# Performance work log

Hardware: AMD Instinct MI355X
Metric: run time of the kernel (lower is better)

Reference implementation:

```python
import jax, jax.numpy as jnp
import numpy as np

NUM_HEADS = 8


def setup_inputs() -> dict:
    key = jax.random.key(0)
    ks = jax.random.split(key, 8)
    B, C, H, W = 8, 512, 64, 64
    s = 1.0 / np.sqrt(C)
    return {
        "guide": jax.random.normal(ks[0], (B, C), dtype=jnp.float32),
        "hidden_rep": jax.random.normal(ks[1], (B, C, H, W), dtype=jnp.float32),
        "Wq": jax.random.normal(ks[2], (C, C), dtype=jnp.float32) * s,
        "bq": jnp.zeros((C,), dtype=jnp.float32),
        "Wk": jax.random.normal(ks[3], (C, C), dtype=jnp.float32) * s,
        "bk": jnp.zeros((C,), dtype=jnp.float32),
        "Wv": jax.random.normal(ks[4], (C, C), dtype=jnp.float32) * s,
        "bv": jnp.zeros((C,), dtype=jnp.float32),
    }


def reference(guide, hidden_rep, Wq, bq, Wk, bk, Wv, bv):
    B, C, H, W = hidden_rep.shape
    nh = NUM_HEADS
    d = C // nh
    scale = 1.0 / (d ** 0.5)

    # hidden_rep: [B,C,H,W] -> [B, HW, C] (token-major, matching torch permute+reshape)
    hr = hidden_rep.transpose(0, 2, 3, 1).reshape(B, H * W, C)

    # guide is broadcast identically over all HW positions in the original;
    # the linear commutes with the broadcast, so compute once then broadcast.
    q_row = guide @ Wq.T + bq                                   # [B, C]
    q_tok = jnp.broadcast_to(q_row[:, None, :], (B, H * W, C))  # [B, HW, C]
    k_tok = hr @ Wk.T + bk                                      # [B, HW, C]
    v_tok = hr @ Wv.T + bv                                      # [B, HW, C]

    # Faithful replication of torch split_heads: view [B,HW,C] as [B,nh,d,H,W]
    # (this scrambles spatial/channel axes exactly as the original does),
    # then permute to [B, nh, H, W, d].
    def split_heads(x):
        return x.reshape(B, nh, d, H, W).transpose(0, 1, 3, 4, 2)

    q = split_heads(q_tok)  # [B, nh, H, W, d]
    k = split_heads(k_tok)
    v = split_heads(v_tok)

    # Row-wise attention: softmax over the width axis only.
    scores = jnp.einsum('bnhqd,bnhkd->bnhqk', q, k) * scale  # [B, nh, H, W, W]
    weights = jax.nn.softmax(scores, axis=-1)
    attended = jnp.einsum('bnhqk,bnhkd->bnhqd', weights, v)  # [B, nh, H, W, d]

    # permute(0,1,4,2,3) -> [B, nh, d, H, W] -> [B, C, H, W]
    return attended.transpose(0, 1, 4, 2, 3).reshape(B, C, H, W)
```

## Files before the change

kernel.cpp:

```cpp
#include <hip/hip_runtime.h>
#include <hip/hip_bf16.h>
#include <stdint.h>


typedef __attribute__((ext_vector_type(8))) short bf16x8_t;
typedef __attribute__((ext_vector_type(4))) float f32x4_t;

__device__ __forceinline__ unsigned short f2bf(float f) {
  unsigned int u = __float_as_uint(f);
  u += 0x7FFFu + ((u >> 16) & 1u);
  return (unsigned short)(u >> 16);
}

__device__ __forceinline__ void gload16(const void* g, void* lds) {
  __builtin_amdgcn_global_load_lds(
      (const __attribute__((address_space(1))) unsigned int*)g,
      (__attribute__((address_space(3))) unsigned int*)lds, 16, 0, 0);
}

__global__ __launch_bounds__(256) void k_trans(const float* __restrict__ hid,
                                               unsigned short* __restrict__ XT,
                                               float* __restrict__ hrsum,
                                               const float* __restrict__ Wv,
                                               unsigned short* __restrict__ Wvb) {
  int bid = blockIdx.x;
  int tid = threadIdx.x;
  if (bid >= 1024) {
    int blk = bid - 1024;
#pragma unroll
    for (int i = 0; i < 16; ++i) {
      int idx = blk * 4096 + i * 256 + tid;
      float4 v = ((const float4*)Wv)[idx];
      ushort4 o;
      o.x = f2bf(v.x); o.y = f2bf(v.y); o.z = f2bf(v.z); o.w = f2bf(v.w);
      ((ushort4*)Wvb)[idx] = o;
    }
    return;
  }
  int rh = bid & 1, cb = (bid >> 1) & 7, n = (bid >> 4) & 7, b = bid >> 7;
  __shared__ float T[32][65];
  __shared__ float hsred[32][8];
  ((float*)hsred)[tid] = 0.f;

  float part[2][4];
#pragma unroll
  for (int m = 0; m < 2; ++m)
#pragma unroll
    for (int i = 0; i < 4; ++i) part[m][i] = 0.f;

  const int f4 = tid & 15;
  const int r0 = tid >> 4;
  const float* srcbase = hid + (size_t)(b * 512 + cb * 64 + rh * 32) * 4096 + n * 512;
  unsigned short* xtbase =
      XT + (size_t)(b * 8 + n) * 512 * 512 + cb * 64 + rh * 32;

  float4 va[2], vb2[2];
#pragma unroll
  for (int m = 0; m < 2; ++m)
    va[m] = *(const float4*)(srcbase + (size_t)(r0 + 16 * m) * 4096 + f4 * 4);

#define TSTEP(JC, CUR, NXT, LAST)                                              \
  do {                                                                         \
    _Pragma("unroll")                                                          \
    for (int m_ = 0; m_ < 2; ++m_) {                                           \
      int r_ = r0 + 16 * m_;                                                   \
      T[r_][f4 * 4 + 0] = CUR[m_].x;  T[r_][f4 * 4 + 1] = CUR[m_].y;           \
      T[r_][f4 * 4 + 2] = CUR[m_].z;  T[r_][f4 * 4 + 3] = CUR[m_].w;           \
      part[m_][0] += CUR[m_].x; part[m_][1] += CUR[m_].y;                      \
      part[m_][2] += CUR[m_].z; part[m_][3] += CUR[m_].w;                      \
    }                                                                          \
    if (!(LAST)) {                                                             \
      _Pragma("unroll")                                                        \
      for (int m_ = 0; m_ < 2; ++m_)                                           \
        NXT[m_] = *(const float4*)(srcbase + (size_t)(r0 + 16 * m_) * 4096 +   \
                                   ((JC) + 1) * 64 + f4 * 4);                  \
    }                                                                          \
    __syncthreads();                                                           \
    {                                                                          \
      int jl_ = tid >> 2, o_ = tid & 3;                                        \
      unsigned short t0 = f2bf(T[o_ * 8 + 0][jl_]);                            \
      unsigned short t1 = f2bf(T[o_ * 8 + 1][jl_]);                            \
      unsigned short t2 = f2bf(T[o_ * 8 + 2][jl_]);                            \
      unsigned short t3 = f2bf(T[o_ * 8 + 3][jl_]);                            \
      unsigned short t4 = f2bf(T[o_ * 8 + 4][jl_]);                            \
      unsigned short t5 = f2bf(T[o_ * 8 + 5][jl_]);                            \
      unsigned short t6 = f2bf(T[o_ * 8 + 6][jl_]);                            \
      unsigned short t7 = f2bf(T[o_ * 8 + 7][jl_]);                            \
      uint4 pk_;                                                               \
      pk_.x = (unsigned)t0 | ((unsigned)t1 << 16);                             \
      pk_.y = (unsigned)t2 | ((unsigned)t3 << 16);                             \
      pk_.z = (unsigned)t4 | ((unsigned)t5 << 16);                             \
      pk_.w = (unsigned)t6 | ((unsigned)t7 << 16);                             \
      *(uint4*)(xtbase + (size_t)((JC) * 64 + jl_) * 512 + o_ * 8) = pk_;      \
    }                                                                          \
    __syncthreads();                                                           \
  } while (0)

  TSTEP(0, va, vb2, 0);
  TSTEP(1, vb2, va, 0);
  TSTEP(2, va, vb2, 0);
  TSTEP(3, vb2, va, 0);
  TSTEP(4, va, vb2, 0);
  TSTEP(5, vb2, va, 0);
  TSTEP(6, va, vb2, 0);
  TSTEP(7, vb2, va, 1);
#undef TSTEP

  {
    int gbase = (f4 & 1) * 4;
#pragma unroll
    for (int m = 0; m < 2; ++m) {
      int r = r0 + 16 * m;
#pragma unroll
      for (int i = 0; i < 4; ++i) atomicAdd(&hsred[r][gbase + i], part[m][i]);
    }
  }
  __syncthreads();
  float* hout = hrsum + (size_t)(b * 8 + n) * 4096 + cb * 64 + rh * 32;
  {
    int g = tid >> 5, r = tid & 31;
    hout[(size_t)g * 512 + r] = hsred[r][g];
  }
}

__global__ __launch_bounds__(256) void k_k2(const float* __restrict__ hrsum,
                                            const float* __restrict__ Wk,
                                            const float* __restrict__ bk,
                                            const float* __restrict__ guide,
                                            const float* __restrict__ Wq,
                                            const float* __restrict__ bq,
                                            float* __restrict__ K2,
                                            float* __restrict__ qs) {
  int bid = blockIdx.x;
  int rt = bid >> 4, ct = bid & 15;
  bool isQ = (rt == 16);
  const float* A = isQ ? guide : (hrsum + (size_t)rt * 32 * 512);
  const float* Bm = isQ ? Wq : Wk;
  int arows = isQ ? 8 : 32;
  int tid = threadIdx.x;
  __shared__ float Ah[32][36];
  __shared__ float Bh[32][36];
  int r = tid >> 3, f = tid & 7;
  int oy = (tid >> 4) * 2, ox = (tid & 15) * 2;
  float a00 = 0.f, a01 = 0.f, a10 = 0.f, a11 = 0.f;

  for (int kc = 0; kc < 16; ++kc) {
    __syncthreads();
    float4 av = (r < arows) ? *(const float4*)(A + (size_t)r * 512 + kc * 32 + f * 4)
                            : make_float4(0.f, 0.f, 0.f, 0.f);
    *(float4*)(&Ah[r][f * 4]) = av;
    float4 bv = *(const float4*)(Bm + (size_t)(ct * 32 + r) * 512 + kc * 32 + f * 4);
    *(float4*)(&Bh[r][f * 4]) = bv;
    __syncthreads();
#pragma unroll
    for (int kk = 0; kk < 32; kk += 4) {
      float4 x0 = *(float4*)(&Ah[oy][kk]);
      float4 x1 = *(float4*)(&Ah[oy + 1][kk]);
      float4 y0 = *(float4*)(&Bh[ox][kk]);
      float4 y1 = *(float4*)(&Bh[ox + 1][kk]);
      a00 += x0.x * y0.x + x0.y * y0.y + x0.z * y0.z + x0.w * y0.w;
      a01 += x0.x * y1.x + x0.y * y1.y + x0.z * y1.z + x0.w * y1.w;
      a10 += x1.x * y0.x + x1.y * y0.y + x1.z * y0.z + x1.w * y0.w;
      a11 += x1.x * y1.x + x1.y * y1.y + x1.z * y1.z + x1.w * y1.w;
    }
  }
  int c0 = ct * 32 + ox;
  if (!isQ) {
    int row0 = rt * 32 + oy;
    K2[(size_t)row0 * 512 + c0]           = a00 + 64.f * bk[c0];
    K2[(size_t)row0 * 512 + c0 + 1]       = a01 + 64.f * bk[c0 + 1];
    K2[(size_t)(row0 + 1) * 512 + c0]     = a10 + 64.f * bk[c0];
    K2[(size_t)(row0 + 1) * 512 + c0 + 1] = a11 + 64.f * bk[c0 + 1];
  } else if (oy < 8) {
    const float scale = 0.125f;
    qs[(size_t)oy * 512 + c0]           = (a00 + bq[c0]) * scale;
    qs[(size_t)oy * 512 + c0 + 1]       = (a01 + bq[c0 + 1]) * scale;
    qs[(size_t)(oy + 1) * 512 + c0]     = (a10 + bq[c0]) * scale;
    qs[(size_t)(oy + 1) * 512 + c0 + 1] = (a11 + bq[c0 + 1]) * scale;
  }
}

__global__ __launch_bounds__(512, 4) void k_fused(
    const unsigned short* __restrict__ XT, const unsigned short* __restrict__ Wvb,
    const float* __restrict__ K2, const float* __restrict__ qs,
    const float* __restrict__ bv, float* __restrict__ out) {
  int p = blockIdx.x;
  int xcd = p & 7, idx = p >> 3;
  int slab = xcd * 8 + (idx & 7);
  int g = idx >> 3;
  int n = slab & 7, b = slab >> 3;

  int tid = threadIdx.x;
  int w = tid >> 6, l = tid & 63;
  int l15 = l & 15, l4 = l >> 4, lr = l >> 3, lc = l & 7;

  __shared__ __align__(16) unsigned char smem[65536];

  const unsigned swzel = (unsigned)((lc ^ lr) << 3);
  const unsigned short* bsrc = XT + (size_t)slab * 512 * 512;
  const unsigned short* wbase = Wvb + (size_t)(w * 64 + l15) * 512 + l4 * 8;
  const int brow = 8 * (w * 8 + lr) + g;

#pragma unroll
  for (int i = 0; i < 8; ++i)
    gload16(bsrc + (size_t)brow * 512 + i * 64 + swzel, smem + i * 8192 + w * 1024);

  float alpha = qs[(size_t)b * 512 + w * 64 + l];
  float beta  = K2[(size_t)(slab * 8 + g) * 512 + w * 64 + l];
  float bvreg = bv[w * 64 + l];

  f32x4_t acc[4][4];
#pragma unroll
  for (int i = 0; i < 4; ++i)
#pragma unroll
    for (int j = 0; j < 4; ++j) acc[i][j] = (f32x4_t){0.f, 0.f, 0.f, 0.f};

  __syncthreads();

#pragma unroll
  for (int s = 0; s < 16; ++s) {
    bf16x8_t af[4];
#pragma unroll
    for (int mt = 0; mt < 4; ++mt)
      af[mt] = *(const bf16x8_t*)(wbase + mt * 16 * 512 + s * 32);
    unsigned char* Bb = smem + (s >> 1) * 8192;
    bf16x8_t bfr[4];
#pragma unroll
    for (int nt = 0; nt < 4; ++nt) {
      unsigned row = (unsigned)(nt * 16 + l15);
      bfr[nt] = *(const bf16x8_t*)(Bb + row * 128 +
                ((unsigned)((s & 1) * 64 + l4 * 16) ^ ((row & 7) << 4)));
    }
    __builtin_amdgcn_s_setprio(1);
#pragma unroll
    for (int mt = 0; mt < 4; ++mt)
#pragma unroll
      for (int nt = 0; nt < 4; ++nt)
        acc[mt][nt] = __builtin_amdgcn_mfma_f32_16x16x32_bf16(
            af[mt], bfr[nt], acc[mt][nt], 0, 0, 0);
    __builtin_amdgcn_s_setprio(0);
  }

  __syncthreads();

  unsigned char* Vp = smem + w * 8192;
#pragma unroll
  for (int mt = 0; mt < 4; ++mt) {
    float bq0 = __shfl(bvreg, mt * 16 + l4 * 4 + 0);
    float bq1 = __shfl(bvreg, mt * 16 + l4 * 4 + 1);
    float bq2 = __shfl(bvreg, mt * 16 + l4 * 4 + 2);
    float bq3 = __shfl(bvreg, mt * 16 + l4 * 4 + 3);
#pragma unroll
    for (int nt = 0; nt < 4; ++nt) {
      unsigned dd = (unsigned)(nt * 16 + l15);
      uint2 pk;
      pk.x = (unsigned)f2bf(acc[mt][nt][0] + bq0) |
             ((unsigned)f2bf(acc[mt][nt][1] + bq1) << 16);
      pk.y = (unsigned)f2bf(acc[mt][nt][2] + bq2) |
             ((unsigned)f2bf(acc[mt][nt][3] + bq3) << 16);
      *(uint2*)(Vp + dd * 128 +
                ((unsigned)(mt * 32 + l4 * 8) ^ ((dd & 7) << 4))) = pk;
    }
  }

  float bmax = beta, bmin = beta;
#pragma unroll
  for (int o = 32; o >= 1; o >>= 1) {
    bmax = fmaxf(bmax, __shfl_xor(bmax, o));
    bmin = fminf(bmin, __shfl_xor(bmin, o));
  }
  float m = alpha >= 0.f ? alpha * bmax : alpha * bmin;
  float ssum = 0.f;
#pragma unroll 8
  for (int kk = 0; kk < 64; ++kk)
    ssum += __expf(fmaf(alpha, __shfl(beta, kk), -m));
  float inv = 1.0f / ssum;

  f32x4_t acc2[4][4];
#pragma unroll
  for (int i = 0; i < 4; ++i)
#pragma unroll
    for (int j = 0; j < 4; ++j) acc2[i][j] = (f32x4_t){0.f, 0.f, 0.f, 0.f};

#pragma unroll
  for (int ks = 0; ks < 2; ++ks) {
    bf16x8_t va[4];
#pragma unroll
    for (int mt = 0; mt < 4; ++mt) {
      unsigned dd = (unsigned)(mt * 16 + l15);
      va[mt] = *(const bf16x8_t*)(Vp + dd * 128 +
                ((unsigned)(ks * 64 + l4 * 16) ^ ((dd & 7) << 4)));
    }
    float bvv[8];
#pragma unroll
    for (int i = 0; i < 8; ++i) bvv[i] = __shfl(beta, ks * 32 + l4 * 8 + i);
    bf16x8_t pb[4];
#pragma unroll
    for (int nt = 0; nt < 4; ++nt) {
      int qq = nt * 16 + l15;
      float aq = __shfl(alpha, qq);
      float mq = __shfl(m, qq);
      float iq = __shfl(inv, qq);
      bf16x8_t pp;
#pragma unroll
      for (int i = 0; i < 8; ++i)
        pp[i] = (short)f2bf(__expf(fmaf(aq, bvv[i], -mq)) * iq);
      pb[nt] = pp;
    }
#pragma unroll
    for (int mt = 0; mt < 4; ++mt)
#pragma unroll
      for (int nt = 0; nt < 4; ++nt)
        acc2[mt][nt] = __builtin_amdgcn_mfma_f32_16x16x32_bf16(
            va[mt], pb[nt], acc2[mt][nt], 0, 0, 0);
  }

#pragma unroll
  for (int mt = 0; mt < 4; ++mt) {
#pragma unroll
    for (int r = 0; r < 4; ++r) {
      int dd = mt * 16 + l4 * 4 + r;
      size_t base = (((size_t)(b * 512 + n * 64 + dd)) * 64 + (g * 8 + w)) * 64;
#pragma unroll
      for (int nt = 0; nt < 4; ++nt)
        out[base + nt * 16 + l15] = acc2[mt][nt][r];
    }
  }
}

extern "C" void kernel_launch(void* const* d_in, const int* in_sizes, int n_in,
                              void* d_out, int out_size, void* d_ws, size_t ws_size,
                              hipStream_t stream) {
  const float* guide = (const float*)d_in[0];
  const float* hid   = (const float*)d_in[1];
  const float* Wq    = (const float*)d_in[2];
  const float* bq    = (const float*)d_in[3];
  const float* Wk    = (const float*)d_in[4];
  const float* bk    = (const float*)d_in[5];
  const float* Wv    = (const float*)d_in[6];
  const float* bv    = (const float*)d_in[7];
  float* out = (float*)d_out;

  char* ws = (char*)d_ws;
  unsigned short* XT  = (unsigned short*)(ws);
  unsigned short* Wvb = (unsigned short*)(ws + 33554432);
  float* hrsum        = (float*)(ws + 34078720);
  float* K2           = (float*)(ws + 35127296);
  float* qs           = (float*)(ws + 36175872);

  k_trans<<<1040, 256, 0, stream>>>(hid, XT, hrsum, Wv, Wvb);
  k_k2<<<272, 256, 0, stream>>>(hrsum, Wk, bk, guide, Wq, bq, K2, qs);
  k_fused<<<512, 512, 0, stream>>>(XT, Wvb, K2, qs, bv, out);
}
```

Before: 94.70 us.

## Precompute softmax probability matrix in separate kernel and double-buffer weight loads

```diff
diff --git a/kernel.cpp b/kernel.cpp
--- a/kernel.cpp
+++ b/kernel.cpp
@@ -180,10 +180,58 @@
   }
 }
 
+__global__ __launch_bounds__(512) void k_pmat(const float* __restrict__ K2,
+                                              const float* __restrict__ qs,
+                                              unsigned short* __restrict__ P) {
+  int p = blockIdx.x;
+  int slab = p >> 3, g = p & 7;
+  int b = slab >> 3;
+  int tid = threadIdx.x;
+  int w = tid >> 6, l = tid & 63;
+
+  float alpha = qs[(size_t)b * 512 + w * 64 + l];
+  float beta  = K2[(size_t)(slab * 8 + g) * 512 + w * 64 + l];
+
+  float bmax = beta, bmin = beta;
+#pragma unroll
+  for (int o = 32; o >= 1; o >>= 1) {
+    bmax = fmaxf(bmax, __shfl_xor(bmax, o));
+    bmin = fminf(bmin, __shfl_xor(bmin, o));
+  }
+  float m = alpha >= 0.f ? alpha * bmax : alpha * bmin;
+  float ssum = 0.f;
+#pragma unroll 8
+  for (int kk = 0; kk < 64; ++kk)
+    ssum += __expf(fmaf(alpha, __shfl(beta, kk), -m));
+  float inv = 1.0f / ssum;
+
+  unsigned short* Pb = P + (((size_t)(slab * 8 + g)) * 8 + w) * 4096;
+  const int qrow = l >> 3, koff = (l & 7) * 8;
+#pragma unroll
+  for (int p8 = 0; p8 < 8; ++p8) {
+    int qq = p8 * 8 + qrow;
+    float aq = __shfl(alpha, qq);
+    float mq = __shfl(m, qq);
+    float iq = __shfl(inv, qq);
+    unsigned short v[8];
+#pragma unroll
+    for (int i = 0; i < 8; ++i) {
+      float bk = __shfl(beta, koff + i);
+      v[i] = f2bf(__expf(fmaf(aq, bk, -mq)) * iq);
+    }
+    uint4 pk;
+    pk.x = (unsigned)v[0] | ((unsigned)v[1] << 16);
+    pk.y = (unsigned)v[2] | ((unsigned)v[3] << 16);
+    pk.z = (unsigned)v[4] | ((unsigned)v[5] << 16);
+    pk.w = (unsigned)v[6] | ((unsigned)v[7] << 16);
+    *(uint4*)(Pb + qq * 64 + koff) = pk;
+  }
+}
+
 __global__ __launch_bounds__(512, 4) void k_fused(
     const unsigned short* __restrict__ XT, const unsigned short* __restrict__ Wvb,
-    const float* __restrict__ K2, const float* __restrict__ qs,
-    const float* __restrict__ bv, float* __restrict__ out) {
+    const unsigned short* __restrict__ P, const float* __restrict__ bv,
+    float* __restrict__ out) {
   int p = blockIdx.x;
   int xcd = p & 7, idx = p >> 3;
   int slab = xcd * 8 + (idx & 7);
@@ -205,8 +253,6 @@
   for (int i = 0; i < 8; ++i)
     gload16(bsrc + (size_t)brow * 512 + i * 64 + swzel, smem + i * 8192 + w * 1024);
 
-  float alpha = qs[(size_t)b * 512 + w * 64 + l];
-  float beta  = K2[(size_t)(slab * 8 + g) * 512 + w * 64 + l];
   float bvreg = bv[w * 64 + l];
 
   f32x4_t acc[4][4];
@@ -217,12 +263,19 @@
 
   __syncthreads();
 
+  bf16x8_t af[2][4];
+#pragma unroll
+  for (int mt = 0; mt < 4; ++mt)
+    af[0][mt] = *(const bf16x8_t*)(wbase + mt * 16 * 512);
+
 #pragma unroll
   for (int s = 0; s < 16; ++s) {
-    bf16x8_t af[4];
-#pragma unroll
-    for (int mt = 0; mt < 4; ++mt)
-      af[mt] = *(const bf16x8_t*)(wbase + mt * 16 * 512 + s * 32);
+    if (s < 15) {
+#pragma unroll
+      for (int mt = 0; mt < 4; ++mt)
+        af[(s + 1) & 1][mt] =
+            *(const bf16x8_t*)(wbase + mt * 16 * 512 + (s + 1) * 32);
+    }
     unsigned char* Bb = smem + (s >> 1) * 8192;
     bf16x8_t bfr[4];
 #pragma unroll
@@ -231,15 +284,21 @@
       bfr[nt] = *(const bf16x8_t*)(Bb + row * 128 +
                 ((unsigned)((s & 1) * 64 + l4 * 16) ^ ((row & 7) << 4)));
     }
-    __builtin_amdgcn_s_setprio(1);
 #pragma unroll
     for (int mt = 0; mt < 4; ++mt)
 #pragma unroll
       for (int nt = 0; nt < 4; ++nt)
         acc[mt][nt] = __builtin_amdgcn_mfma_f32_16x16x32_bf16(
-            af[mt], bfr[nt], acc[mt][nt], 0, 0, 0);
-    __builtin_amdgcn_s_setprio(0);
-  }
+            af[s & 1][mt], bfr[nt], acc[mt][nt], 0, 0, 0);
+  }
+
+  const unsigned short* Pb = P + (((size_t)(slab * 8 + g)) * 8 + w) * 4096;
+  bf16x8_t pb[2][4];
+#pragma unroll
+  for (int ks = 0; ks < 2; ++ks)
+#pragma unroll
+    for (int nt = 0; nt < 4; ++nt)
+      pb[ks][nt] = *(const bf16x8_t*)(Pb + (nt * 16 + l15) * 64 + ks * 32 + l4 * 8);
 
   __syncthreads();
 
@@ -263,19 +322,6 @@
     }
   }
 
-  float bmax = beta, bmin = beta;
-#pragma unroll
-  for (int o = 32; o >= 1; o >>= 1) {
-    bmax = fmaxf(bmax, __shfl_xor(bmax, o));
-    bmin = fminf(bmin, __shfl_xor(bmin, o));
-  }
-  float m = alpha >= 0.f ? alpha * bmax : alpha * bmin;
-  float ssum = 0.f;
-#pragma unroll 8
-  for (int kk = 0; kk < 64; ++kk)
-    ssum += __expf(fmaf(alpha, __shfl(beta, kk), -m));
-  float inv = 1.0f / ssum;
-
   f32x4_t acc2[4][4];
 #pragma unroll
   for (int i = 0; i < 4; ++i)
@@ -291,28 +337,12 @@
       va[mt] = *(const bf16x8_t*)(Vp + dd * 128 +
                 ((unsigned)(ks * 64 + l4 * 16) ^ ((dd & 7) << 4)));
     }
-    float bvv[8];
-#pragma unroll
-    for (int i = 0; i < 8; ++i) bvv[i] = __shfl(beta, ks * 32 + l4 * 8 + i);
-    bf16x8_t pb[4];
-#pragma unroll
-    for (int nt = 0; nt < 4; ++nt) {
-      int qq = nt * 16 + l15;
-      float aq = __shfl(alpha, qq);
-      float mq = __shfl(m, qq);
-      float iq = __shfl(inv, qq);
-      bf16x8_t pp;
-#pragma unroll
-      for (int i = 0; i < 8; ++i)
-        pp[i] = (short)f2bf(__expf(fmaf(aq, bvv[i], -mq)) * iq);
-      pb[nt] = pp;
-    }
 #pragma unroll
     for (int mt = 0; mt < 4; ++mt)
 #pragma unroll
       for (int nt = 0; nt < 4; ++nt)
         acc2[mt][nt] = __builtin_amdgcn_mfma_f32_16x16x32_bf16(
-            va[mt], pb[nt], acc2[mt][nt], 0, 0, 0);
+            va[mt], pb[ks][nt], acc2[mt][nt], 0, 0, 0);
   }
 
 #pragma unroll
@@ -347,8 +377,10 @@
   float* hrsum        = (float*)(ws + 34078720);
   float* K2           = (float*)(ws + 35127296);
   float* qs           = (float*)(ws + 36175872);
+  unsigned short* P   = (unsigned short*)(ws + 36192256);
 
   k_trans<<<1040, 256, 0, stream>>>(hid, XT, hrsum, Wv, Wvb);
   k_k2<<<272, 256, 0, stream>>>(hrsum, Wk, bk, guide, Wq, bq, K2, qs);
-  k_fused<<<512, 512, 0, stream>>>(XT, Wvb, K2, qs, bv, out);
-}
+  k_pmat<<<512, 512, 0, stream>>>(K2, qs, P);
+  k_fused<<<512, 512, 0, stream>>>(XT, Wvb, P, bv, out);
+}
```

New measurement: 108.5 us. 1.15x slower.

## Process two head slabs per fused block to reuse Wv fragments

Applied to the files above, without the earlier changes.

```diff
diff --git a/kernel.cpp b/kernel.cpp
--- a/kernel.cpp
+++ b/kernel.cpp
@@ -180,152 +180,183 @@
   }
 }
 
-__global__ __launch_bounds__(512, 4) void k_fused(
+__global__ __launch_bounds__(512, 2) void k_fused(
     const unsigned short* __restrict__ XT, const unsigned short* __restrict__ Wvb,
     const float* __restrict__ K2, const float* __restrict__ qs,
     const float* __restrict__ bv, float* __restrict__ out) {
   int p = blockIdx.x;
   int xcd = p & 7, idx = p >> 3;
-  int slab = xcd * 8 + (idx & 7);
-  int g = idx >> 3;
-  int n = slab & 7, b = slab >> 3;
+  int sp = xcd * 4 + (idx & 3);
+  int g = idx >> 2;
+  int slab0 = sp * 2, slab1 = slab0 + 1;
+  int b = sp >> 2;
+  int n0 = slab0 & 7, n1 = slab1 & 7;
 
   int tid = threadIdx.x;
   int w = tid >> 6, l = tid & 63;
   int l15 = l & 15, l4 = l >> 4, lr = l >> 3, lc = l & 7;
 
-  __shared__ __align__(16) unsigned char smem[65536];
+  __shared__ __align__(16) unsigned char smem[131072];
 
   const unsigned swzel = (unsigned)((lc ^ lr) << 3);
-  const unsigned short* bsrc = XT + (size_t)slab * 512 * 512;
+  const unsigned short* xsrc0 = XT + (size_t)slab0 * 512 * 512;
+  const unsigned short* xsrc1 = XT + (size_t)slab1 * 512 * 512;
   const unsigned short* wbase = Wvb + (size_t)(w * 64 + l15) * 512 + l4 * 8;
   const int brow = 8 * (w * 8 + lr) + g;
 
 #pragma unroll
   for (int i = 0; i < 8; ++i)
-    gload16(bsrc + (size_t)brow * 512 + i * 64 + swzel, smem + i * 8192 + w * 1024);
+    gload16(xsrc0 + (size_t)brow * 512 + i * 64 + swzel,
+            smem + i * 8192 + w * 1024);
+#pragma unroll
+  for (int i = 0; i < 8; ++i)
+    gload16(xsrc1 + (size_t)brow * 512 + i * 64 + swzel,
+            smem + 65536 + i * 8192 + w * 1024);
 
   float alpha = qs[(size_t)b * 512 + w * 64 + l];
-  float beta  = K2[(size_t)(slab * 8 + g) * 512 + w * 64 + l];
+  float beta0 = K2[(size_t)(slab0 * 8 + g) * 512 + w * 64 + l];
+  float beta1 = K2[(size_t)(slab1 * 8 + g) * 512 + w * 64 + l];
   float bvreg = bv[w * 64 + l];
 
-  f32x4_t acc[4][4];
+  f32x4_t acc0[4][4], acc1[4][4];
 #pragma unroll
   for (int i = 0; i < 4; ++i)
 #pragma unroll
-    for (int j = 0; j < 4; ++j) acc[i][j] = (f32x4_t){0.f, 0.f, 0.f, 0.f};
+    for (int j = 0; j < 4; ++j) {
+      acc0[i][j] = (f32x4_t){0.f, 0.f, 0.f, 0.f};
+      acc1[i][j] = (f32x4_t){0.f, 0.f, 0.f, 0.f};
+    }
 
   __syncthreads();
 
+  bf16x8_t af[2][4];
+#pragma unroll
+  for (int mt = 0; mt < 4; ++mt)
+    af[0][mt] = *(const bf16x8_t*)(wbase + mt * 16 * 512);
+
 #pragma unroll
   for (int s = 0; s < 16; ++s) {
-    bf16x8_t af[4];
-#pragma unroll
-    for (int mt = 0; mt < 4; ++mt)
-      af[mt] = *(const bf16x8_t*)(wbase + mt * 16 * 512 + s * 32);
-    unsigned char* Bb = smem + (s >> 1) * 8192;
-    bf16x8_t bfr[4];
+    if (s < 15) {
+#pragma unroll
+      for (int mt = 0; mt < 4; ++mt)
+        af[(s + 1) & 1][mt] =
+            *(const bf16x8_t*)(wbase + mt * 16 * 512 + (s + 1) * 32);
+    }
+    unsigned colx = (unsigned)((s & 1) * 64 + l4 * 16);
+    unsigned char* Ba = smem + (s >> 1) * 8192;
+    unsigned char* Bb = smem + 65536 + (s >> 1) * 8192;
+    bf16x8_t b0[4], b1[4];
 #pragma unroll
     for (int nt = 0; nt < 4; ++nt) {
       unsigned row = (unsigned)(nt * 16 + l15);
-      bfr[nt] = *(const bf16x8_t*)(Bb + row * 128 +
-                ((unsigned)((s & 1) * 64 + l4 * 16) ^ ((row & 7) << 4)));
-    }
-    __builtin_amdgcn_s_setprio(1);
+      unsigned off = row * 128 + (colx ^ ((row & 7) << 4));
+      b0[nt] = *(const bf16x8_t*)(Ba + off);
+      b1[nt] = *(const bf16x8_t*)(Bb + off);
+    }
 #pragma unroll
     for (int mt = 0; mt < 4; ++mt)
 #pragma unroll
       for (int nt = 0; nt < 4; ++nt)
-        acc[mt][nt] = __builtin_amdgcn_mfma_f32_16x16x32_bf16(
-            af[mt], bfr[nt], acc[mt][nt], 0, 0, 0);
-    __builtin_amdgcn_s_setprio(0);
+        acc0[mt][nt] = __builtin_amdgcn_mfma_f32_16x16x32_bf16(
+            af[s & 1][mt], b0[nt], acc0[mt][nt], 0, 0, 0);
+#pragma unroll
+    for (int mt = 0; mt < 4; ++mt)
+#pragma unroll
+      for (int nt = 0; nt < 4; ++nt)
+        acc1[mt][nt] = __builtin_amdgcn_mfma_f32_16x16x32_bf16(
+            af[s & 1][mt], b1[nt], acc1[mt][nt], 0, 0, 0);
   }
 
   __syncthreads();
 
-  unsigned char* Vp = smem + w * 8192;
-#pragma unroll
-  for (int mt = 0; mt < 4; ++mt) {
-    float bq0 = __shfl(bvreg, mt * 16 + l4 * 4 + 0);
-    float bq1 = __shfl(bvreg, mt * 16 + l4 * 4 + 1);
-    float bq2 = __shfl(bvreg, mt * 16 + l4 * 4 + 2);
-    float bq3 = __shfl(bvreg, mt * 16 + l4 * 4 + 3);
-#pragma unroll
-    for (int nt = 0; nt < 4; ++nt) {
-      unsigned dd = (unsigned)(nt * 16 + l15);
-      uint2 pk;
-      pk.x = (unsigned)f2bf(acc[mt][nt][0] + bq0) |
-             ((unsigned)f2bf(acc[mt][nt][1] + bq1) << 16);
-      pk.y = (unsigned)f2bf(acc[mt][nt][2] + bq2) |
-             ((unsigned)f2bf(acc[mt][nt][3] + bq3) << 16);
-      *(uint2*)(Vp + dd * 128 +
-                ((unsigned)(mt * 32 + l4 * 8) ^ ((dd & 7) << 4))) = pk;
-    }
-  }
-
-  float bmax = beta, bmin = beta;
-#pragma unroll
-  for (int o = 32; o >= 1; o >>= 1) {
-    bmax = fmaxf(bmax, __shfl_xor(bmax, o));
-    bmin = fminf(bmin, __shfl_xor(bmin, o));
-  }
-  float m = alpha >= 0.f ? alpha * bmax : alpha * bmin;
-  float ssum = 0.f;
-#pragma unroll 8
-  for (int kk = 0; kk < 64; ++kk)
-    ssum += __expf(fmaf(alpha, __shfl(beta, kk), -m));
-  float inv = 1.0f / ssum;
-
-  f32x4_t acc2[4][4];
-#pragma unroll
-  for (int i = 0; i < 4; ++i)
-#pragma unroll
-    for (int j = 0; j < 4; ++j) acc2[i][j] = (f32x4_t){0.f, 0.f, 0.f, 0.f};
-
-#pragma unroll
-  for (int ks = 0; ks < 2; ++ks) {
-    bf16x8_t va[4];
-#pragma unroll
-    for (int mt = 0; mt < 4; ++mt) {
-      unsigned dd = (unsigned)(mt * 16 + l15);
-      va[mt] = *(const bf16x8_t*)(Vp + dd * 128 +
-                ((unsigned)(ks * 64 + l4 * 16) ^ ((dd & 7) << 4)));
-    }
-    float bvv[8];
-#pragma unroll
-    for (int i = 0; i < 8; ++i) bvv[i] = __shfl(beta, ks * 32 + l4 * 8 + i);
-    bf16x8_t pb[4];
-#pragma unroll
-    for (int nt = 0; nt < 4; ++nt) {
-      int qq = nt * 16 + l15;
-      float aq = __shfl(alpha, qq);
-      float mq = __shfl(m, qq);
-      float iq = __shfl(inv, qq);
-      bf16x8_t pp;
-#pragma unroll
-      for (int i = 0; i < 8; ++i)
-        pp[i] = (short)f2bf(__expf(fmaf(aq, bvv[i], -mq)) * iq);
-      pb[nt] = pp;
-    }
-#pragma unroll
-    for (int mt = 0; mt < 4; ++mt)
-#pragma unroll
-      for (int nt = 0; nt < 4; ++nt)
-        acc2[mt][nt] = __builtin_amdgcn_mfma_f32_16x16x32_bf16(
-            va[mt], pb[nt], acc2[mt][nt], 0, 0, 0);
-  }
-
-#pragma unroll
-  for (int mt = 0; mt < 4; ++mt) {
-#pragma unroll
-    for (int r = 0; r < 4; ++r) {
-      int dd = mt * 16 + l4 * 4 + r;
-      size_t base = (((size_t)(b * 512 + n * 64 + dd)) * 64 + (g * 8 + w)) * 64;
-#pragma unroll
-      for (int nt = 0; nt < 4; ++nt)
-        out[base + nt * 16 + l15] = acc2[mt][nt][r];
-    }
-  }
+#define SLAB_TAIL(ACC, VPOFF, BETA, NN)                                        \
+  do {                                                                         \
+    unsigned char* Vp = smem + (VPOFF) + w * 8192;                             \
+    _Pragma("unroll")                                                          \
+    for (int mt = 0; mt < 4; ++mt) {                                           \
+      float bq0 = __shfl(bvreg, mt * 16 + l4 * 4 + 0);                         \
+      float bq1 = __shfl(bvreg, mt * 16 + l4 * 4 + 1);                         \
+      float bq2 = __shfl(bvreg, mt * 16 + l4 * 4 + 2);                         \
+      float bq3 = __shfl(bvreg, mt * 16 + l4 * 4 + 3);                         \
+      _Pragma("unroll")                                                        \
+      for (int nt = 0; nt < 4; ++nt) {                                         \
+        unsigned dd = (unsigned)(nt * 16 + l15);                               \
+        uint2 pk;                                                              \
+        pk.x = (unsigned)f2bf(ACC[mt][nt][0] + bq0) |                          \
+               ((unsigned)f2bf(ACC[mt][nt][1] + bq1) << 16);                   \
+        pk.y = (unsigned)f2bf(ACC[mt][nt][2] + bq2) |                          \
+               ((unsigned)f2bf(ACC[mt][nt][3] + bq3) << 16);                   \
+        *(uint2*)(Vp + dd * 128 +                                              \
+                  ((unsigned)(mt * 32 + l4 * 8) ^ ((dd & 7) << 4))) = pk;      \
+      }                                                                        \
+    }                                                                          \
+    float bmax = (BETA), bmin = (BETA);                                        \
+    _Pragma("unroll")                                                          \
+    for (int o = 32; o >= 1; o >>= 1) {                                        \
+      bmax = fmaxf(bmax, __shfl_xor(bmax, o));                                 \
+      bmin = fminf(bmin, __shfl_xor(bmin, o));                                 \
+    }                                                                          \
+    float m = alpha >= 0.f ? alpha * bmax : alpha * bmin;                      \
+    float ssum = 0.f;                                                          \
+    _Pragma("unroll 8")                                                        \
+    for (int kk = 0; kk < 64; ++kk)                                            \
+      ssum += __expf(fmaf(alpha, __shfl((BETA), kk), -m));                     \
+    float inv = 1.0f / ssum;                                                   \
+    f32x4_t acc2[4][4];                                                        \
+    _Pragma("unroll")                                                          \
+    for (int i = 0; i < 4; ++i)                                                \
+      _Pragma("unroll")                                                        \
+      for (int j = 0; j < 4; ++j) acc2[i][j] = (f32x4_t){0.f, 0.f, 0.f, 0.f};  \
+    _Pragma("unroll")                                                          \
+    for (int ks = 0; ks < 2; ++ks) {                                           \
+      bf16x8_t va[4];                                                          \
+      _Pragma("unroll")                                                        \
+      for (int mt = 0; mt < 4; ++mt) {                                         \
+        unsigned dd = (unsigned)(mt * 16 + l15);                               \
+        va[mt] = *(const bf16x8_t*)(Vp + dd * 128 +                            \
+                  ((unsigned)(ks * 64 + l4 * 16) ^ ((dd & 7) << 4)));          \
+      }                                                                        \
+      float bvv[8];                                                            \
+      _Pragma("unroll")                                                        \
+      for (int i = 0; i < 8; ++i)                                              \
+        bvv[i] = __shfl((BETA), ks * 32 + l4 * 8 + i);                         \
+      bf16x8_t pb[4];                                                          \
+      _Pragma("unroll")                                                        \
+      for (int nt = 0; nt < 4; ++nt) {                                         \
+        int qq = nt * 16 + l15;                                                \
+        float aq = __shfl(alpha, qq);                                          \
+        float mq = __shfl(m, qq);                                              \
+        float iq = __shfl(inv, qq);                                            \
+        bf16x8_t pp;                                                           \
+        _Pragma("unroll")                                                      \
+        for (int i = 0; i < 8; ++i)                                            \
+          pp[i] = (short)f2bf(__expf(fmaf(aq, bvv[i], -mq)) * iq);             \
+        pb[nt] = pp;                                                           \
+      }                                                                        \
+      _Pragma("unroll")                                                        \
+      for (int mt = 0; mt < 4; ++mt)                                           \
+        _Pragma("unroll")                                                      \
+        for (int nt = 0; nt < 4; ++nt)                                         \
+          acc2[mt][nt] = __builtin_amdgcn_mfma_f32_16x16x32_bf16(              \
+              va[mt], pb[nt], acc2[mt][nt], 0, 0, 0);                          \
+    }                                                                          \
+    _Pragma("unroll")                                                          \
+    for (int mt = 0; mt < 4; ++mt) {                                           \
+      _Pragma("unroll")                                                        \
+      for (int r = 0; r < 4; ++r) {                                            \
+        int dd = mt * 16 + l4 * 4 + r;                                         \
+        size_t base =                                                          \
+            (((size_t)(b * 512 + (NN) * 64 + dd)) * 64 + (g * 8 + w)) * 64;    \
+        _Pragma("unroll")                                                      \
+        for (int nt = 0; nt < 4; ++nt)                                         \
+          out[base + nt * 16 + l15] = acc2[mt][nt][r];                         \
+      }                                                                        \
+    }                                                                          \
+  } while (0)
+
+  SLAB_TAIL(acc0, 0, beta0, n0);
+  SLAB_TAIL(acc1, 65536, beta1, n1);
+#undef SLAB_TAIL
 }
 
 extern "C" void kernel_launch(void* const* d_in, const int* in_sizes, int n_in,
@@ -350,5 +381,5 @@
 
   k_trans<<<1040, 256, 0, stream>>>(hid, XT, hrsum, Wv, Wvb);
   k_k2<<<272, 256, 0, stream>>>(hrsum, Wk, bk, guide, Wq, bq, K2, qs);
-  k_fused<<<512, 512, 0, stream>>>(XT, Wvb, K2, qs, bv, out);
-}
+  k_fused<<<256, 512, 0, stream>>>(XT, Wvb, K2, qs, bv, out);
+}
```

Result: faster. 84.20 us (-11.1%).

## Split fused attention into single-wave blocks loading operands directly from global

Applied to the files above, without the earlier changes.

```diff
diff --git a/kernel.cpp b/kernel.cpp
--- a/kernel.cpp
+++ b/kernel.cpp
@@ -10,12 +10,6 @@
   unsigned int u = __float_as_uint(f);
   u += 0x7FFFu + ((u >> 16) & 1u);
   return (unsigned short)(u >> 16);
-}
-
-__device__ __forceinline__ void gload16(const void* g, void* lds) {
-  __builtin_amdgcn_global_load_lds(
-      (const __attribute__((address_space(1))) unsigned int*)g,
-      (__attribute__((address_space(3))) unsigned int*)lds, 16, 0, 0);
 }
 
 __global__ __launch_bounds__(256) void k_trans(const float* __restrict__ hid,
@@ -180,70 +174,66 @@
   }
 }
 
-__global__ __launch_bounds__(512, 4) void k_fused(
+__global__ __launch_bounds__(64, 4) void k_attn(
     const unsigned short* __restrict__ XT, const unsigned short* __restrict__ Wvb,
     const float* __restrict__ K2, const float* __restrict__ qs,
     const float* __restrict__ bv, float* __restrict__ out) {
   int p = blockIdx.x;
-  int xcd = p & 7, idx = p >> 3;
-  int slab = xcd * 8 + (idx & 7);
-  int g = idx >> 3;
-  int n = slab & 7, b = slab >> 3;
-
-  int tid = threadIdx.x;
-  int w = tid >> 6, l = tid & 63;
-  int l15 = l & 15, l4 = l >> 4, lr = l >> 3, lc = l & 7;
-
-  __shared__ __align__(16) unsigned char smem[65536];
-
-  const unsigned swzel = (unsigned)((lc ^ lr) << 3);
-  const unsigned short* bsrc = XT + (size_t)slab * 512 * 512;
-  const unsigned short* wbase = Wvb + (size_t)(w * 64 + l15) * 512 + l4 * 8;
-  const int brow = 8 * (w * 8 + lr) + g;
-
-#pragma unroll
-  for (int i = 0; i < 8; ++i)
-    gload16(bsrc + (size_t)brow * 512 + i * 64 + swzel, smem + i * 8192 + w * 1024);
-
-  float alpha = qs[(size_t)b * 512 + w * 64 + l];
-  float beta  = K2[(size_t)(slab * 8 + g) * 512 + w * 64 + l];
-  float bvreg = bv[w * 64 + l];
+  int xcd = p & 7, i = p >> 3;
+  int slab = xcd * 8 + (i >> 6);
+  int rem = i & 63;
+  int g = rem >> 3, e = rem & 7;
+  int b = slab >> 3, n = slab & 7;
+
+  int l = threadIdx.x;
+  int l15 = l & 15, l4 = l >> 4;
+
+  __shared__ __align__(16) unsigned char Vp[8192];
+
+  const unsigned short* xbase =
+      XT + (size_t)slab * 262144 + (size_t)l15 * 4096 + g * 512 + l4 * 8;
+  const unsigned short* wbase = Wvb + (size_t)(e * 64 + l15) * 512 + l4 * 8;
+
+  float alpha = qs[(size_t)b * 512 + e * 64 + l];
+  float beta  = K2[(size_t)(slab * 8 + g) * 512 + e * 64 + l];
+  float bvreg = bv[e * 64 + l];
+
+  float bmax = beta, bmin = beta;
+#pragma unroll
+  for (int o = 32; o >= 1; o >>= 1) {
+    bmax = fmaxf(bmax, __shfl_xor(bmax, o));
+    bmin = fminf(bmin, __shfl_xor(bmin, o));
+  }
+  float m = alpha >= 0.f ? alpha * bmax : alpha * bmin;
+  float ssum = 0.f;
+#pragma unroll 8
+  for (int kk = 0; kk < 64; ++kk)
+    ssum += __expf(fmaf(alpha, __shfl(beta, kk), -m));
+  float inv = 1.0f / ssum;
 
   f32x4_t acc[4][4];
 #pragma unroll
-  for (int i = 0; i < 4; ++i)
-#pragma unroll
-    for (int j = 0; j < 4; ++j) acc[i][j] = (f32x4_t){0.f, 0.f, 0.f, 0.f};
-
-  __syncthreads();
+  for (int mi = 0; mi < 4; ++mi)
+#pragma unroll
+    for (int j = 0; j < 4; ++j) acc[mi][j] = (f32x4_t){0.f, 0.f, 0.f, 0.f};
 
 #pragma unroll
   for (int s = 0; s < 16; ++s) {
-    bf16x8_t af[4];
+    bf16x8_t af[4], bf[4];
 #pragma unroll
     for (int mt = 0; mt < 4; ++mt)
       af[mt] = *(const bf16x8_t*)(wbase + mt * 16 * 512 + s * 32);
-    unsigned char* Bb = smem + (s >> 1) * 8192;
-    bf16x8_t bfr[4];
-#pragma unroll
-    for (int nt = 0; nt < 4; ++nt) {
-      unsigned row = (unsigned)(nt * 16 + l15);
-      bfr[nt] = *(const bf16x8_t*)(Bb + row * 128 +
-                ((unsigned)((s & 1) * 64 + l4 * 16) ^ ((row & 7) << 4)));
-    }
-    __builtin_amdgcn_s_setprio(1);
+#pragma unroll
+    for (int nt = 0; nt < 4; ++nt)
+      bf[nt] = *(const bf16x8_t*)(xbase + (size_t)nt * 65536 + s * 32);
 #pragma unroll
     for (int mt = 0; mt < 4; ++mt)
 #pragma unroll
       for (int nt = 0; nt < 4; ++nt)
         acc[mt][nt] = __builtin_amdgcn_mfma_f32_16x16x32_bf16(
-            af[mt], bfr[nt], acc[mt][nt], 0, 0, 0);
-    __builtin_amdgcn_s_setprio(0);
-  }
-
-  __syncthreads();
-
-  unsigned char* Vp = smem + w * 8192;
+            af[mt], bf[nt], acc[mt][nt], 0, 0, 0);
+  }
+
 #pragma unroll
   for (int mt = 0; mt < 4; ++mt) {
     float bq0 = __shfl(bvreg, mt * 16 + l4 * 4 + 0);
@@ -263,67 +253,54 @@
     }
   }
 
-  float bmax = beta, bmin = beta;
-#pragma unroll
-  for (int o = 32; o >= 1; o >>= 1) {
-    bmax = fmaxf(bmax, __shfl_xor(bmax, o));
-    bmin = fminf(bmin, __shfl_xor(bmin, o));
-  }
-  float m = alpha >= 0.f ? alpha * bmax : alpha * bmin;
-  float ssum = 0.f;
-#pragma unroll 8
-  for (int kk = 0; kk < 64; ++kk)
-    ssum += __expf(fmaf(alpha, __shfl(beta, kk), -m));
-  float inv = 1.0f / ssum;
-
   f32x4_t acc2[4][4];
 #pragma unroll
-  for (int i = 0; i < 4; ++i)
-#pragma unroll
-    for (int j = 0; j < 4; ++j) acc2[i][j] = (f32x4_t){0.f, 0.f, 0.f, 0.f};
+  for (int mi = 0; mi < 4; ++mi)
+#pragma unroll
+    for (int j = 0; j < 4; ++j) acc2[mi][j] = (f32x4_t){0.f, 0.f, 0.f, 0.f};
 
 #pragma unroll
   for (int ks = 0; ks < 2; ++ks) {
     bf16x8_t va[4];
 #pragma unroll
+    for (int nt = 0; nt < 4; ++nt) {
+      unsigned dd = (unsigned)(nt * 16 + l15);
+      va[nt] = *(const bf16x8_t*)(Vp + dd * 128 +
+                ((unsigned)(ks * 64 + l4 * 16) ^ ((dd & 7) << 4)));
+    }
+    float bb[8];
+#pragma unroll
+    for (int i2 = 0; i2 < 8; ++i2) bb[i2] = __shfl(beta, ks * 32 + l4 * 8 + i2);
+    bf16x8_t pa[4];
+#pragma unroll
     for (int mt = 0; mt < 4; ++mt) {
-      unsigned dd = (unsigned)(mt * 16 + l15);
-      va[mt] = *(const bf16x8_t*)(Vp + dd * 128 +
-                ((unsigned)(ks * 64 + l4 * 16) ^ ((dd & 7) << 4)));
-    }
-    float bvv[8];
-#pragma unroll
-    for (int i = 0; i < 8; ++i) bvv[i] = __shfl(beta, ks * 32 + l4 * 8 + i);
-    bf16x8_t pb[4];
-#pragma unroll
-    for (int nt = 0; nt < 4; ++nt) {
-      int qq = nt * 16 + l15;
+      int qq = mt * 16 + l15;
       float aq = __shfl(alpha, qq);
       float mq = __shfl(m, qq);
       float iq = __shfl(inv, qq);
       bf16x8_t pp;
 #pragma unroll
-      for (int i = 0; i < 8; ++i)
-        pp[i] = (short)f2bf(__expf(fmaf(aq, bvv[i], -mq)) * iq);
-      pb[nt] = pp;
+      for (int i2 = 0; i2 < 8; ++i2)
+        pp[i2] = (short)f2bf(__expf(fmaf(aq, bb[i2], -mq)) * iq);
+      pa[mt] = pp;
     }
 #pragma unroll
     for (int mt = 0; mt < 4; ++mt)
 #pragma unroll
       for (int nt = 0; nt < 4; ++nt)
         acc2[mt][nt] = __builtin_amdgcn_mfma_f32_16x16x32_bf16(
-            va[mt], pb[nt], acc2[mt][nt], 0, 0, 0);
-  }
-
-#pragma unroll
-  for (int mt = 0; mt < 4; ++mt) {
-#pragma unroll
-    for (int r = 0; r < 4; ++r) {
-      int dd = mt * 16 + l4 * 4 + r;
-      size_t base = (((size_t)(b * 512 + n * 64 + dd)) * 64 + (g * 8 + w)) * 64;
-#pragma unroll
-      for (int nt = 0; nt < 4; ++nt)
-        out[base + nt * 16 + l15] = acc2[mt][nt][r];
+            pa[mt], va[nt], acc2[mt][nt], 0, 0, 0);
+  }
+
+#pragma unroll
+  for (int nt = 0; nt < 4; ++nt) {
+    int dd = nt * 16 + l15;
+    size_t base = (((size_t)(b * 512 + n * 64 + dd)) * 64 + (g * 8 + e)) * 64;
+#pragma unroll
+    for (int mt = 0; mt < 4; ++mt) {
+      float4 v = make_float4(acc2[mt][nt][0], acc2[mt][nt][1],
+                             acc2[mt][nt][2], acc2[mt][nt][3]);
+      *(float4*)(out + base + mt * 16 + l4 * 4) = v;
     }
   }
 }
@@ -350,5 +327,5 @@
 
   k_trans<<<1040, 256, 0, stream>>>(hid, XT, hrsum, Wv, Wvb);
   k_k2<<<272, 256, 0, stream>>>(hrsum, Wk, bk, guide, Wq, bq, K2, qs);
-  k_fused<<<512, 512, 0, stream>>>(XT, Wvb, K2, qs, bv, out);
-}
+  k_attn<<<4096, 64, 0, stream>>>(XT, Wvb, K2, qs, bv, out);
+}
```

Result: slower. 117.7 us (+24.3%).
